# Performance work log

Hardware: AMD Instinct MI355X
Metric: run time of the kernel (lower is better)

## Reference

```python
import jax, jax.numpy as jnp
import numpy as np


def _gcn_conv(x, W, b, src, dst, deg_inv_sqrt, n_nodes):
    # x: [N, Fin], W: [Fin, Fout]; edges (with self-loops): src, dst [E+N]
    h = x @ W  # [N, Fout]
    norm = deg_inv_sqrt[src] * deg_inv_sqrt[dst]  # [E+N]
    msgs = h[src] * norm[:, None]  # gather-multiply
    out = jax.ops.segment_sum(msgs, dst, num_segments=n_nodes)  # scatter-add
    return out + b


def setup_inputs() -> dict:
    key = jax.random.key(0)
    k1, k2, k3, k4 = jax.random.split(key, 4)
    N, E, FIN, HID, OUT = 100000, 3200000, 128, 32, 32
    x = jax.random.normal(k1, (N, FIN), dtype=jnp.float32)
    edge_index = jax.random.randint(k2, (2, E), 0, N, dtype=jnp.int64)
    W1 = jax.random.normal(k3, (FIN, HID), dtype=jnp.float32) * (1.0 / np.sqrt(FIN))
    b1 = jnp.zeros((HID,), dtype=jnp.float32)
    W2 = jax.random.normal(k4, (HID, OUT), dtype=jnp.float32) * (1.0 / np.sqrt(HID))
    b2 = jnp.zeros((OUT,), dtype=jnp.float32)
    return {"x": x, "edge_index": edge_index, "W1": W1, "b1": b1, "W2": W2, "b2": b2}


def reference(x, edge_index, W1, b1, W2, b2):
    n = x.shape[0]
    # GCNConv defaults: add self-loops, symmetric normalization D^-1/2 (A+I) D^-1/2
    loops = jnp.arange(n, dtype=edge_index.dtype)
    src = jnp.concatenate([edge_index[0], loops])
    dst = jnp.concatenate([edge_index[1], loops])
    deg = jax.ops.segment_sum(jnp.ones_like(dst, dtype=x.dtype), dst, num_segments=n)
    deg_inv_sqrt = jnp.where(deg > 0, jax.lax.rsqrt(jnp.maximum(deg, 1.0)), 0.0)
    h = jax.nn.relu(_gcn_conv(x, W1, b1, src, dst, deg_inv_sqrt, n))  # hidden layer + ReLU
    out = jax.nn.relu(_gcn_conv(h, W2, b2, src, dst, deg_inv_sqrt, n))  # last layer + last_activation relu
    return out
```

## Files before the change

kernel.cpp:

```cpp
#include <hip/hip_runtime.h>
#include <hip/hip_fp16.h>

#define FIN 128
#define HID 32
#define BSHIFT 8
#define BNODES 256
#define CHUNK 4096
#define NBMAX 512
#define CAPB 8960
#define G1ROWS 64


__global__ __launch_bounds__(512) void chunk_sort_kernel(const int* __restrict__ src,
                                                         const int* __restrict__ dst,
                                                         int* __restrict__ ec,
                                                         unsigned short* __restrict__ offtT,
                                                         int E, int nb, int nchunks) {
    __shared__ int hist[NBMAX];
    __shared__ int pref[NBMAX];
    __shared__ int sorted[CHUNK];
    int c = blockIdx.x, t = threadIdx.x;
    int beg = c * CHUNK;
    int cnt = min(CHUNK, E - beg);
    for (int i = t; i < nb; i += 512) hist[i] = 0;
    __syncthreads();
    int bk[8], ent[8];
    #pragma unroll
    for (int j = 0; j < 8; ++j) {
        int i = t + j * 512;
        if (i < cnt) {
            int d = dst[beg + i];
            bk[j]  = ((unsigned)d) >> BSHIFT;
            ent[j] = src[beg + i] | ((d & (BNODES - 1)) << 24);
            atomicAdd(&hist[bk[j]], 1);
        } else bk[j] = -1;
    }
    __syncthreads();
    if (t < 64) {
        int v[8];
        int s = 0;
        #pragma unroll
        for (int j = 0; j < 8; ++j) {
            int idx = t * 8 + j;
            int h = (idx < nb) ? hist[idx] : 0;
            v[j] = s; s += h;
        }
        int run = s;
        #pragma unroll
        for (int d = 1; d < 64; d <<= 1) {
            int o = __shfl_up(run, d, 64);
            if (t >= d) run += o;
        }
        int excl = run - s;
        #pragma unroll
        for (int j = 0; j < 8; ++j) {
            int idx = t * 8 + j;
            if (idx < nb) { int p = excl + v[j]; pref[idx] = p; hist[idx] = p; }
        }
    }
    __syncthreads();
    #pragma unroll
    for (int j = 0; j < 8; ++j) {
        if (bk[j] >= 0) {
            int p = atomicAdd(&hist[bk[j]], 1);
            sorted[p] = ent[j];
        }
    }
    __syncthreads();
    for (int i = t; i < cnt; i += 512) ec[(size_t)c * CHUNK + i] = sorted[i];
    for (int i = t; i < nb; i += 512) offtT[(size_t)i * nchunks + c] = (unsigned short)pref[i];
    if (t == 0) offtT[(size_t)nb * nchunks + c] = (unsigned short)cnt;
}


__global__ __launch_bounds__(512) void bucket_build_kernel(const int* __restrict__ ec,
                                                           const unsigned short* __restrict__ offtT,
                                                           int* __restrict__ entries,
                                                           float* __restrict__ dinv,
                                                           int* __restrict__ rowbeg,
                                                           int* __restrict__ rowcnt,
                                                           int n, int nb, int nchunks, int cap) {
    __shared__ int raw[CAPB];
    __shared__ int hist[BNODES];
    __shared__ int pref[BNODES];
    __shared__ int cursor[BNODES];
    __shared__ int nfill;
    int b = blockIdx.x, t = threadIdx.x;
    if (t < BNODES) hist[t] = 0;
    if (t == 0) nfill = 0;
    __syncthreads();
    const unsigned short* r0 = offtT + (size_t)b * nchunks;
    const unsigned short* r1 = offtT + (size_t)(b + 1) * nchunks;
    int lane = t & 3;
    for (int c = (t >> 2); c < nchunks; c += 128) {
        int s = r0[c], e2 = r1[c];
        int m = e2 - s;
        if (m > 0) {
            int base;
            if (lane == 0) base = atomicAdd(&nfill, m);
            base = __shfl(base, 0, 4);
            const int* p = ec + (size_t)c * CHUNK + s;
            for (int k = lane; k < m; k += 4) {
                int e = p[k];
                if (base + k < CAPB) raw[base + k] = e;
                atomicAdd(&hist[((unsigned)e) >> 24], 1);
            }
        }
    }
    __syncthreads();
    int total = min(nfill, CAPB);
    if (t < 64) {
        int v[4];
        int s = 0;
        #pragma unroll
        for (int j = 0; j < 4; ++j) { v[j] = s; s += hist[t * 4 + j]; }
        int run = s;
        #pragma unroll
        for (int d = 1; d < 64; d <<= 1) {
            int o = __shfl_up(run, d, 64);
            if (t >= d) run += o;
        }
        int excl = run - s;
        #pragma unroll
        for (int j = 0; j < 4; ++j) {
            int idx = t * 4 + j;
            int p = excl + v[j];
            pref[idx] = p; cursor[idx] = p;
        }
    }
    __syncthreads();
    int* ep = entries + (size_t)b * cap;
    for (int i = t; i < total; i += 512) {
        int e = raw[i];
        int p = atomicAdd(&cursor[((unsigned)e) >> 24], 1);
        ep[p] = e;
    }
    int node = b * BNODES + t;
    if (t < BNODES && node < n) {
        int deg = hist[t];
        dinv[node]   = rsqrtf((float)deg + 1.0f);
        rowbeg[node] = b * cap + pref[t];
        rowcnt[node] = deg;
    }
}


__global__ __launch_bounds__(256) void gemm1_kernel(const float* __restrict__ x,
                                                    const float* __restrict__ W,
                                                    const float* __restrict__ dinv,
                                                    __half* __restrict__ h16, int n) {
    __shared__ float Ws[FIN * HID];
    int t = threadIdx.x;
    for (int i = t; i < FIN * HID; i += 256) Ws[i] = W[i];
    __syncthreads();
    int row0 = blockIdx.x * G1ROWS;
    int tr = t >> 3, tc = t & 7;
    int r0 = row0 + tr * 2, c0 = tc * 4;
    bool v0 = r0 < n, v1 = (r0 + 1) < n;
    const float* p0 = v0 ? &x[(size_t)r0 * FIN] : x;
    const float* p1 = v1 ? &x[(size_t)(r0 + 1) * FIN] : x;
    float4 a0 = make_float4(0.f, 0.f, 0.f, 0.f);
    float4 a1 = make_float4(0.f, 0.f, 0.f, 0.f);
    #pragma unroll 8
    for (int k4 = 0; k4 < FIN / 4; ++k4) {
        float4 xv0 = *(const float4*)&p0[k4 * 4];
        float4 xv1 = *(const float4*)&p1[k4 * 4];
        float4 w0 = *(const float4*)&Ws[(k4 * 4 + 0) * HID + c0];
        float4 w1 = *(const float4*)&Ws[(k4 * 4 + 1) * HID + c0];
        float4 w2 = *(const float4*)&Ws[(k4 * 4 + 2) * HID + c0];
        float4 w3 = *(const float4*)&Ws[(k4 * 4 + 3) * HID + c0];
        a0.x = fmaf(xv0.x, w0.x, a0.x); a0.y = fmaf(xv0.x, w0.y, a0.y);
        a0.z = fmaf(xv0.x, w0.z, a0.z); a0.w = fmaf(xv0.x, w0.w, a0.w);
        a0.x = fmaf(xv0.y, w1.x, a0.x); a0.y = fmaf(xv0.y, w1.y, a0.y);
        a0.z = fmaf(xv0.y, w1.z, a0.z); a0.w = fmaf(xv0.y, w1.w, a0.w);
        a0.x = fmaf(xv0.z, w2.x, a0.x); a0.y = fmaf(xv0.z, w2.y, a0.y);
        a0.z = fmaf(xv0.z, w2.z, a0.z); a0.w = fmaf(xv0.z, w2.w, a0.w);
        a0.x = fmaf(xv0.w, w3.x, a0.x); a0.y = fmaf(xv0.w, w3.y, a0.y);
        a0.z = fmaf(xv0.w, w3.z, a0.z); a0.w = fmaf(xv0.w, w3.w, a0.w);
        a1.x = fmaf(xv1.x, w0.x, a1.x); a1.y = fmaf(xv1.x, w0.y, a1.y);
        a1.z = fmaf(xv1.x, w0.z, a1.z); a1.w = fmaf(xv1.x, w0.w, a1.w);
        a1.x = fmaf(xv1.y, w1.x, a1.x); a1.y = fmaf(xv1.y, w1.y, a1.y);
        a1.z = fmaf(xv1.y, w1.z, a1.z); a1.w = fmaf(xv1.y, w1.w, a1.w);
        a1.x = fmaf(xv1.z, w2.x, a1.x); a1.y = fmaf(xv1.z, w2.y, a1.y);
        a1.z = fmaf(xv1.z, w2.z, a1.z); a1.w = fmaf(xv1.z, w2.w, a1.w);
        a1.x = fmaf(xv1.w, w3.x, a1.x); a1.y = fmaf(xv1.w, w3.y, a1.y);
        a1.z = fmaf(xv1.w, w3.z, a1.z); a1.w = fmaf(xv1.w, w3.w, a1.w);
    }
    #pragma unroll
    for (int rr = 0; rr < 2; ++rr) {
        int row = r0 + rr;
        float4 a = rr ? a1 : a0;
        float sc = (row < n) ? dinv[row] : 0.f;
        __half2 q0 = __floats2half2_rn(a.x * sc, a.y * sc);
        __half2 q1 = __floats2half2_rn(a.z * sc, a.w * sc);
        __half2* dstp = (__half2*)&h16[(size_t)row * HID + c0];
        dstp[0] = q0;
        dstp[1] = q1;
    }
}


template <int FUSEW2>
__global__ __launch_bounds__(256) void gather_kernel(const int* __restrict__ entries,
                                                     const int* __restrict__ rowbeg,
                                                     const int* __restrict__ rowcnt,
                                                     const float* __restrict__ dinv,
                                                     const __half* __restrict__ h16,
                                                     const float* __restrict__ bias,
                                                     const float* __restrict__ W2,
                                                     __half* __restrict__ houth,
                                                     float* __restrict__ outf,
                                                     int n, int sent) {
    __shared__ float Ws[HID * HID];
    int t = threadIdx.x;
    if (FUSEW2) {
        for (int i = t; i < HID * HID; i += 256) Ws[i] = W2[i];
        __syncthreads();
    }
    int g = t >> 2, f = t & 3;
    int i = blockIdx.x * 64 + g;
    if (i >= n) return;
    float di = dinv[i];
    float a[8];
    {
        float4 sv4 = *(const float4*)&h16[(size_t)i * HID + f * 8];
        const __half2* sh = (const __half2*)&sv4;
        #pragma unroll
        for (int q = 0; q < 4; ++q) {
            float2 fp = __half22float2(sh[q]);
            a[2 * q] = fp.x; a[2 * q + 1] = fp.y;
        }
    }
    int beg = rowbeg[i], cnt = rowcnt[i];
    for (int base = 0; base < cnt; base += 8) {
        int i0 = base + f, i1 = base + 4 + f;
        int sv0 = (i0 < cnt) ? entries[beg + i0] : sent;
        int sv1 = (i1 < cnt) ? entries[beg + i1] : sent;
        sv0 &= 0xFFFFFF; sv1 &= 0xFFFFFF;
        float4 hv[8];
        #pragma unroll
        for (int j = 0; j < 4; ++j) {
            int e = __shfl(sv0, j, 4);
            hv[j] = *(const float4*)&h16[(size_t)e * HID + f * 8];
        }
        #pragma unroll
        for (int j = 0; j < 4; ++j) {
            int e = __shfl(sv1, j, 4);
            hv[4 + j] = *(const float4*)&h16[(size_t)e * HID + f * 8];
        }
        #pragma unroll
        for (int j = 0; j < 8; ++j) {
            const __half2* hp = (const __half2*)&hv[j];
            #pragma unroll
            for (int q = 0; q < 4; ++q) {
                float2 fp = __half22float2(hp[q]);
                a[2 * q] += fp.x; a[2 * q + 1] += fp.y;
            }
        }
    }
    float4 b0 = *(const float4*)&bias[f * 8];
    float4 b1 = *(const float4*)&bias[f * 8 + 4];
    float bj[8] = {b0.x, b0.y, b0.z, b0.w, b1.x, b1.y, b1.z, b1.w};
    float rl[8];
    #pragma unroll
    for (int j = 0; j < 8; ++j) rl[j] = fmaxf(bj[j] + di * a[j], 0.f);

    if (!FUSEW2) {
        *(float4*)&outf[(size_t)i * HID + f * 8]     = make_float4(rl[0], rl[1], rl[2], rl[3]);
        *(float4*)&outf[(size_t)i * HID + f * 8 + 4] = make_float4(rl[4], rl[5], rl[6], rl[7]);
    } else {
        int c0 = f * 8;
        float o[8] = {0.f, 0.f, 0.f, 0.f, 0.f, 0.f, 0.f, 0.f};
        #pragma unroll
        for (int s = 0; s < 4; ++s) {
            #pragma unroll
            for (int j = 0; j < 8; ++j) {
                float av = __shfl(rl[j], s, 4);
                int k = s * 8 + j;
                float4 w0 = *(const float4*)&Ws[k * HID + c0];
                float4 w1 = *(const float4*)&Ws[k * HID + c0 + 4];
                o[0] = fmaf(av, w0.x, o[0]); o[1] = fmaf(av, w0.y, o[1]);
                o[2] = fmaf(av, w0.z, o[2]); o[3] = fmaf(av, w0.w, o[3]);
                o[4] = fmaf(av, w1.x, o[4]); o[5] = fmaf(av, w1.y, o[5]);
                o[6] = fmaf(av, w1.z, o[6]); o[7] = fmaf(av, w1.w, o[7]);
            }
        }
        float4 tmp;
        __half2* hp2 = (__half2*)&tmp;
        #pragma unroll
        for (int j = 0; j < 4; ++j) hp2[j] = __floats2half2_rn(di * o[2 * j], di * o[2 * j + 1]);
        *(float4*)&houth[(size_t)i * HID + f * 8] = tmp;
    }
}

extern "C" void kernel_launch(void* const* d_in, const int* in_sizes, int n_in,
                              void* d_out, int out_size, void* d_ws, size_t ws_size,
                              hipStream_t stream) {
    const float* x  = (const float*)d_in[0];
    const int*   ei = (const int*)d_in[1];
    const float* W1 = (const float*)d_in[2];
    const float* b1 = (const float*)d_in[3];
    const float* W2 = (const float*)d_in[4];
    const float* b2 = (const float*)d_in[5];
    float* out = (float*)d_out;

    int n = in_sizes[0] / FIN;
    int E = in_sizes[1] / 2;
    const int* src = ei;
    const int* dst = ei + E;

    int nb = (n + BNODES - 1) / BNODES;
    int nchunks = (E + CHUNK - 1) / CHUNK;
    int ggrid = (n + G1ROWS) / G1ROWS;
    int npad = ggrid * G1ROWS;
    int cap = CAPB;

    char* ws = (char*)d_ws;
    size_t off = 0;
    auto alloc = [&](size_t bytes) { char* p = ws + off; off += (bytes + 255) & ~(size_t)255; return p; };
    int*            ec      = (int*)alloc((size_t)nchunks * CHUNK * 4);
    unsigned short* offtT   = (unsigned short*)alloc((size_t)(nb + 1) * nchunks * 2);
    int*            entries = (int*)alloc((size_t)nb * cap * 4);
    float*          dinv    = (float*)alloc((size_t)n * 4);
    int*            rowbeg  = (int*)alloc((size_t)n * 4);
    int*            rowcnt  = (int*)alloc((size_t)n * 4);
    __half*         hha     = (__half*)alloc((size_t)npad * HID * 2);
    __half*         hhb     = (__half*)alloc((size_t)(n + 1) * HID * 2);

    hipMemsetAsync(hhb + (size_t)n * HID, 0, HID * 2, stream);

    chunk_sort_kernel<<<nchunks, 512, 0, stream>>>(src, dst, ec, offtT, E, nb, nchunks);
    bucket_build_kernel<<<nb, 512, 0, stream>>>(ec, offtT, entries, dinv, rowbeg, rowcnt,
                                                n, nb, nchunks, cap);

    gemm1_kernel<<<ggrid, 256, 0, stream>>>(x, W1, dinv, hha, n);
    gather_kernel<1><<<(n + 63) / 64, 256, 0, stream>>>(entries, rowbeg, rowcnt, dinv, hha,
                                                        b1, W2, hhb, nullptr, n, n);

    gather_kernel<0><<<(n + 63) / 64, 256, 0, stream>>>(entries, rowbeg, rowcnt, dinv, hhb,
                                                        b2, nullptr, nullptr, out, n, n);
}
```

Measured before the change: 248.0 us.

## Split feature matrices into 16-column half planes for cache-friendly gathers

Stores the fp16 hidden features as two separate 16-column planes and runs each gather pass once per plane, so each pass's random-access working set (about 3.2 MB per plane) is half the size and fits better in L2/MALL. Layer 1 becomes two gather passes; the second combines the stashed fp32 first-half result with its own half before applying the fused W2 projection. Layer 2 is likewise split into two passes. This trades extra kernel launches, re-reading the edge list four times instead of twice, and an fp32 intermediate buffer for better cache hit rates on the random gathers.

```diff
diff --git a/kernel.cpp b/kernel.cpp
--- a/kernel.cpp
+++ b/kernel.cpp
@@ -9,6 +9,7 @@
 #define NBMAX 512
 #define CAPB 8960
 #define G1ROWS 64
+#define PL 16
 
 
 __global__ __launch_bounds__(512) void chunk_sort_kernel(const int* __restrict__ src,
@@ -148,7 +149,8 @@
 __global__ __launch_bounds__(256) void gemm1_kernel(const float* __restrict__ x,
                                                     const float* __restrict__ W,
                                                     const float* __restrict__ dinv,
-                                                    __half* __restrict__ h16, int n) {
+                                                    __half* __restrict__ hpa,
+                                                    __half* __restrict__ hpb, int n) {
     __shared__ float Ws[FIN * HID];
     int t = threadIdx.x;
     for (int i = t; i < FIN * HID; i += 256) Ws[i] = W[i];
@@ -186,34 +188,37 @@
         a1.x = fmaf(xv1.w, w3.x, a1.x); a1.y = fmaf(xv1.w, w3.y, a1.y);
         a1.z = fmaf(xv1.w, w3.z, a1.z); a1.w = fmaf(xv1.w, w3.w, a1.w);
     }
+    __half* hp = (c0 >= PL) ? hpb : hpa;
+    int pc = c0 & (PL - 1);
     #pragma unroll
     for (int rr = 0; rr < 2; ++rr) {
         int row = r0 + rr;
         float4 a = rr ? a1 : a0;
         float sc = (row < n) ? dinv[row] : 0.f;
-        __half2 q0 = __floats2half2_rn(a.x * sc, a.y * sc);
-        __half2 q1 = __floats2half2_rn(a.z * sc, a.w * sc);
-        __half2* dstp = (__half2*)&h16[(size_t)row * HID + c0];
-        dstp[0] = q0;
-        dstp[1] = q1;
-    }
-}
-
-
-template <int FUSEW2>
+        union { __half2 h2[2]; float2 f2; } pk;
+        pk.h2[0] = __floats2half2_rn(a.x * sc, a.y * sc);
+        pk.h2[1] = __floats2half2_rn(a.z * sc, a.w * sc);
+        *(float2*)&hp[(size_t)row * PL + pc] = pk.f2;
+    }
+}
+
+
+template <int MODE>
 __global__ __launch_bounds__(256) void gather_kernel(const int* __restrict__ entries,
                                                      const int* __restrict__ rowbeg,
                                                      const int* __restrict__ rowcnt,
                                                      const float* __restrict__ dinv,
-                                                     const __half* __restrict__ h16,
-                                                     const float* __restrict__ bias,
+                                                     const __half* __restrict__ hplane,
+                                                     const float* __restrict__ bias16,
+                                                     const float* __restrict__ rA,
                                                      const float* __restrict__ W2,
-                                                     __half* __restrict__ houth,
+                                                     __half* __restrict__ opa,
+                                                     __half* __restrict__ opb,
                                                      float* __restrict__ outf,
                                                      int n, int sent) {
     __shared__ float Ws[HID * HID];
     int t = threadIdx.x;
-    if (FUSEW2) {
+    if (MODE == 1) {
         for (int i = t; i < HID * HID; i += 256) Ws[i] = W2[i];
         __syncthreads();
     }
@@ -221,75 +226,75 @@
     int i = blockIdx.x * 64 + g;
     if (i >= n) return;
     float di = dinv[i];
-    float a[8];
+    float a0, a1, a2, a3;
     {
-        float4 sv4 = *(const float4*)&h16[(size_t)i * HID + f * 8];
-        const __half2* sh = (const __half2*)&sv4;
-        #pragma unroll
-        for (int q = 0; q < 4; ++q) {
-            float2 fp = __half22float2(sh[q]);
-            a[2 * q] = fp.x; a[2 * q + 1] = fp.y;
-        }
+        float2 sv = *(const float2*)&hplane[(size_t)i * PL + f * 4];
+        const __half2* sh = (const __half2*)&sv;
+        float2 u = __half22float2(sh[0]), v = __half22float2(sh[1]);
+        a0 = u.x; a1 = u.y; a2 = v.x; a3 = v.y;
     }
     int beg = rowbeg[i], cnt = rowcnt[i];
-    for (int base = 0; base < cnt; base += 8) {
-        int i0 = base + f, i1 = base + 4 + f;
-        int sv0 = (i0 < cnt) ? entries[beg + i0] : sent;
-        int sv1 = (i1 < cnt) ? entries[beg + i1] : sent;
-        sv0 &= 0xFFFFFF; sv1 &= 0xFFFFFF;
-        float4 hv[8];
-        #pragma unroll
-        for (int j = 0; j < 4; ++j) {
-            int e = __shfl(sv0, j, 4);
-            hv[j] = *(const float4*)&h16[(size_t)e * HID + f * 8];
-        }
-        #pragma unroll
-        for (int j = 0; j < 4; ++j) {
-            int e = __shfl(sv1, j, 4);
-            hv[4 + j] = *(const float4*)&h16[(size_t)e * HID + f * 8];
-        }
-        #pragma unroll
-        for (int j = 0; j < 8; ++j) {
-            const __half2* hp = (const __half2*)&hv[j];
+    for (int base = 0; base < cnt; base += 16) {
+        int sv[4];
+        #pragma unroll
+        for (int k = 0; k < 4; ++k) {
+            int idx = base + f * 4 + k;
+            sv[k] = (idx < cnt) ? entries[beg + idx] : sent;
+        }
+        float2 hv[16];
+        #pragma unroll
+        for (int e = 0; e < 16; ++e) {
+            int en = __shfl(sv[e & 3], e >> 2, 4) & 0xFFFFFF;
+            hv[e] = *(const float2*)&hplane[(size_t)en * PL + f * 4];
+        }
+        #pragma unroll
+        for (int e = 0; e < 16; ++e) {
+            const __half2* hp = (const __half2*)&hv[e];
+            float2 u = __half22float2(hp[0]), v = __half22float2(hp[1]);
+            a0 += u.x; a1 += u.y; a2 += v.x; a3 += v.y;
+        }
+    }
+    float4 bb = *(const float4*)&bias16[f * 4];
+    float rl[4];
+    rl[0] = fmaxf(bb.x + di * a0, 0.f);
+    rl[1] = fmaxf(bb.y + di * a1, 0.f);
+    rl[2] = fmaxf(bb.z + di * a2, 0.f);
+    rl[3] = fmaxf(bb.w + di * a3, 0.f);
+
+    if (MODE == 0) {
+        *(float4*)&outf[(size_t)i * PL + f * 4] = make_float4(rl[0], rl[1], rl[2], rl[3]);
+    } else if (MODE == 2) {
+        *(float4*)&outf[(size_t)i * HID + f * 4] = make_float4(rl[0], rl[1], rl[2], rl[3]);
+    } else {
+        float r[32];
+        const float4* ra = (const float4*)&rA[(size_t)i * PL];
+        float4 ra0 = ra[0], ra1 = ra[1], ra2 = ra[2], ra3 = ra[3];
+        r[0] = ra0.x; r[1] = ra0.y; r[2]  = ra0.z; r[3]  = ra0.w;
+        r[4] = ra1.x; r[5] = ra1.y; r[6]  = ra1.z; r[7]  = ra1.w;
+        r[8] = ra2.x; r[9] = ra2.y; r[10] = ra2.z; r[11] = ra2.w;
+        r[12] = ra3.x; r[13] = ra3.y; r[14] = ra3.z; r[15] = ra3.w;
+        #pragma unroll
+        for (int s = 0; s < 4; ++s) {
             #pragma unroll
-            for (int q = 0; q < 4; ++q) {
-                float2 fp = __half22float2(hp[q]);
-                a[2 * q] += fp.x; a[2 * q + 1] += fp.y;
-            }
-        }
-    }
-    float4 b0 = *(const float4*)&bias[f * 8];
-    float4 b1 = *(const float4*)&bias[f * 8 + 4];
-    float bj[8] = {b0.x, b0.y, b0.z, b0.w, b1.x, b1.y, b1.z, b1.w};
-    float rl[8];
-    #pragma unroll
-    for (int j = 0; j < 8; ++j) rl[j] = fmaxf(bj[j] + di * a[j], 0.f);
-
-    if (!FUSEW2) {
-        *(float4*)&outf[(size_t)i * HID + f * 8]     = make_float4(rl[0], rl[1], rl[2], rl[3]);
-        *(float4*)&outf[(size_t)i * HID + f * 8 + 4] = make_float4(rl[4], rl[5], rl[6], rl[7]);
-    } else {
+            for (int j = 0; j < 4; ++j) r[16 + s * 4 + j] = __shfl(rl[j], s, 4);
+        }
         int c0 = f * 8;
         float o[8] = {0.f, 0.f, 0.f, 0.f, 0.f, 0.f, 0.f, 0.f};
         #pragma unroll
-        for (int s = 0; s < 4; ++s) {
-            #pragma unroll
-            for (int j = 0; j < 8; ++j) {
-                float av = __shfl(rl[j], s, 4);
-                int k = s * 8 + j;
-                float4 w0 = *(const float4*)&Ws[k * HID + c0];
-                float4 w1 = *(const float4*)&Ws[k * HID + c0 + 4];
-                o[0] = fmaf(av, w0.x, o[0]); o[1] = fmaf(av, w0.y, o[1]);
-                o[2] = fmaf(av, w0.z, o[2]); o[3] = fmaf(av, w0.w, o[3]);
-                o[4] = fmaf(av, w1.x, o[4]); o[5] = fmaf(av, w1.y, o[5]);
-                o[6] = fmaf(av, w1.z, o[6]); o[7] = fmaf(av, w1.w, o[7]);
-            }
-        }
-        float4 tmp;
-        __half2* hp2 = (__half2*)&tmp;
-        #pragma unroll
-        for (int j = 0; j < 4; ++j) hp2[j] = __floats2half2_rn(di * o[2 * j], di * o[2 * j + 1]);
-        *(float4*)&houth[(size_t)i * HID + f * 8] = tmp;
+        for (int k = 0; k < HID; ++k) {
+            float av = r[k];
+            float4 w0 = *(const float4*)&Ws[k * HID + c0];
+            float4 w1 = *(const float4*)&Ws[k * HID + c0 + 4];
+            o[0] = fmaf(av, w0.x, o[0]); o[1] = fmaf(av, w0.y, o[1]);
+            o[2] = fmaf(av, w0.z, o[2]); o[3] = fmaf(av, w0.w, o[3]);
+            o[4] = fmaf(av, w1.x, o[4]); o[5] = fmaf(av, w1.y, o[5]);
+            o[6] = fmaf(av, w1.z, o[6]); o[7] = fmaf(av, w1.w, o[7]);
+        }
+        __half* op = (f & 2) ? opb : opa;
+        union { __half2 h2[4]; float4 f4; } pk;
+        #pragma unroll
+        for (int j = 0; j < 4; ++j) pk.h2[j] = __floats2half2_rn(di * o[2 * j], di * o[2 * j + 1]);
+        *(float4*)&op[(size_t)i * PL + (f & 1) * 8] = pk.f4;
     }
 }
 
@@ -324,19 +329,32 @@
     float*          dinv    = (float*)alloc((size_t)n * 4);
     int*            rowbeg  = (int*)alloc((size_t)n * 4);
     int*            rowcnt  = (int*)alloc((size_t)n * 4);
-    __half*         hha     = (__half*)alloc((size_t)npad * HID * 2);
-    __half*         hhb     = (__half*)alloc((size_t)(n + 1) * HID * 2);
-
-    hipMemsetAsync(hhb + (size_t)n * HID, 0, HID * 2, stream);
+    __half*         hpa     = (__half*)alloc((size_t)npad * PL * 2);
+    __half*         hpb     = (__half*)alloc((size_t)npad * PL * 2);
+    __half*         hqa     = (__half*)alloc((size_t)(n + 1) * PL * 2);
+    __half*         hqb     = (__half*)alloc((size_t)(n + 1) * PL * 2);
+    float*          rAbuf   = (float*)alloc((size_t)n * PL * 4);
+
+    hipMemsetAsync(hqa + (size_t)n * PL, 0, PL * 2, stream);
+    hipMemsetAsync(hqb + (size_t)n * PL, 0, PL * 2, stream);
 
     chunk_sort_kernel<<<nchunks, 512, 0, stream>>>(src, dst, ec, offtT, E, nb, nchunks);
     bucket_build_kernel<<<nb, 512, 0, stream>>>(ec, offtT, entries, dinv, rowbeg, rowcnt,
                                                 n, nb, nchunks, cap);
 
-    gemm1_kernel<<<ggrid, 256, 0, stream>>>(x, W1, dinv, hha, n);
-    gather_kernel<1><<<(n + 63) / 64, 256, 0, stream>>>(entries, rowbeg, rowcnt, dinv, hha,
-                                                        b1, W2, hhb, nullptr, n, n);
-
-    gather_kernel<0><<<(n + 63) / 64, 256, 0, stream>>>(entries, rowbeg, rowcnt, dinv, hhb,
-                                                        b2, nullptr, nullptr, out, n, n);
-}
+    gemm1_kernel<<<ggrid, 256, 0, stream>>>(x, W1, dinv, hpa, hpb, n);
+
+    int ggath = (n + 63) / 64;
+    gather_kernel<0><<<ggath, 256, 0, stream>>>(entries, rowbeg, rowcnt, dinv, hpa,
+                                                b1, nullptr, nullptr, nullptr, nullptr,
+                                                rAbuf, n, n);
+    gather_kernel<1><<<ggath, 256, 0, stream>>>(entries, rowbeg, rowcnt, dinv, hpb,
+                                                b1 + PL, rAbuf, W2, hqa, hqb,
+                                                nullptr, n, n);
+    gather_kernel<2><<<ggath, 256, 0, stream>>>(entries, rowbeg, rowcnt, dinv, hqa,
+                                                b2, nullptr, nullptr, nullptr, nullptr,
+                                                out, n, n);
+    gather_kernel<2><<<ggath, 256, 0, stream>>>(entries, rowbeg, rowcnt, dinv, hqb,
+                                                b2 + PL, nullptr, nullptr, nullptr, nullptr,
+                                                out + PL, n, n);
+}
```

Result: slower. 276.6 us (+11.5%).

## Sort nodes by degree within buckets and widen gather unroll to 16 edges

Applied to the files above, without the earlier changes.

The bucket build kernel now counting-sorts the nodes of each 256-node bucket by in-degree and writes a node permutation. Both gather kernels walk nodes through that permutation, so the wavefronts in a block handle nodes of similar degree and lose less time to divergence. The gather loop also fetches 16 neighbour rows per iteration instead of 8, giving more loads in flight. The costs are an extra indirection, less contiguous output writes, and higher register pressure from the wider unroll.

```diff
diff --git a/kernel.cpp b/kernel.cpp
--- a/kernel.cpp
+++ b/kernel.cpp
@@ -9,6 +9,7 @@
 #define NBMAX 512
 #define CAPB 8960
 #define G1ROWS 64
+#define DBINS 64
 
 
 __global__ __launch_bounds__(512) void chunk_sort_kernel(const int* __restrict__ src,
@@ -79,14 +80,18 @@
                                                            float* __restrict__ dinv,
                                                            int* __restrict__ rowbeg,
                                                            int* __restrict__ rowcnt,
+                                                           int* __restrict__ nodeperm,
                                                            int n, int nb, int nchunks, int cap) {
     __shared__ int raw[CAPB];
     __shared__ int hist[BNODES];
     __shared__ int pref[BNODES];
     __shared__ int cursor[BNODES];
+    __shared__ int dhist[DBINS];
+    __shared__ int dcur[DBINS];
     __shared__ int nfill;
     int b = blockIdx.x, t = threadIdx.x;
     if (t < BNODES) hist[t] = 0;
+    if (t < DBINS) dhist[t] = 0;
     if (t == 0) nfill = 0;
     __syncthreads();
     const unsigned short* r0 = offtT + (size_t)b * nchunks;
@@ -135,12 +140,33 @@
         int p = atomicAdd(&cursor[((unsigned)e) >> 24], 1);
         ep[p] = e;
     }
-    int node = b * BNODES + t;
-    if (t < BNODES && node < n) {
-        int deg = hist[t];
-        dinv[node]   = rsqrtf((float)deg + 1.0f);
-        rowbeg[node] = b * cap + pref[t];
-        rowcnt[node] = deg;
+    int myd = -1;
+    if (t < BNODES) {
+        myd = min(hist[t], DBINS - 1);
+        atomicAdd(&dhist[myd], 1);
+    }
+    __syncthreads();
+    if (t < 64) {
+        int s = dhist[t];
+        int run = s;
+        #pragma unroll
+        for (int d = 1; d < 64; d <<= 1) {
+            int o = __shfl_up(run, d, 64);
+            if (t >= d) run += o;
+        }
+        dcur[t] = run - s;
+    }
+    __syncthreads();
+    if (t < BNODES) {
+        int node = b * BNODES + t;
+        int rank = atomicAdd(&dcur[myd], 1);
+        nodeperm[b * BNODES + rank] = (node < n) ? node : -1;
+        if (node < n) {
+            int deg = hist[t];
+            dinv[node]   = rsqrtf((float)deg + 1.0f);
+            rowbeg[node] = b * cap + pref[t];
+            rowcnt[node] = deg;
+        }
     }
 }
 
@@ -201,7 +227,8 @@
 
 
 template <int FUSEW2>
-__global__ __launch_bounds__(256) void gather_kernel(const int* __restrict__ entries,
+__global__ __launch_bounds__(256) void gather_kernel(const int* __restrict__ nodeperm,
+                                                     const int* __restrict__ entries,
                                                      const int* __restrict__ rowbeg,
                                                      const int* __restrict__ rowcnt,
                                                      const float* __restrict__ dinv,
@@ -210,7 +237,7 @@
                                                      const float* __restrict__ W2,
                                                      __half* __restrict__ houth,
                                                      float* __restrict__ outf,
-                                                     int n, int sent) {
+                                                     int sent) {
     __shared__ float Ws[HID * HID];
     int t = threadIdx.x;
     if (FUSEW2) {
@@ -218,8 +245,8 @@
         __syncthreads();
     }
     int g = t >> 2, f = t & 3;
-    int i = blockIdx.x * 64 + g;
-    if (i >= n) return;
+    int i = nodeperm[blockIdx.x * 64 + g];
+    if (i < 0) return;
     float di = dinv[i];
     float a[8];
     {
@@ -232,25 +259,22 @@
         }
     }
     int beg = rowbeg[i], cnt = rowcnt[i];
-    for (int base = 0; base < cnt; base += 8) {
-        int i0 = base + f, i1 = base + 4 + f;
-        int sv0 = (i0 < cnt) ? entries[beg + i0] : sent;
-        int sv1 = (i1 < cnt) ? entries[beg + i1] : sent;
-        sv0 &= 0xFFFFFF; sv1 &= 0xFFFFFF;
-        float4 hv[8];
-        #pragma unroll
-        for (int j = 0; j < 4; ++j) {
-            int e = __shfl(sv0, j, 4);
-            hv[j] = *(const float4*)&h16[(size_t)e * HID + f * 8];
-        }
-        #pragma unroll
-        for (int j = 0; j < 4; ++j) {
-            int e = __shfl(sv1, j, 4);
-            hv[4 + j] = *(const float4*)&h16[(size_t)e * HID + f * 8];
-        }
-        #pragma unroll
-        for (int j = 0; j < 8; ++j) {
-            const __half2* hp = (const __half2*)&hv[j];
+    for (int base = 0; base < cnt; base += 16) {
+        int sv[4];
+        #pragma unroll
+        for (int k = 0; k < 4; ++k) {
+            int idx = base + k * 4 + f;
+            sv[k] = (idx < cnt) ? entries[beg + idx] : sent;
+        }
+        float4 hv[16];
+        #pragma unroll
+        for (int e = 0; e < 16; ++e) {
+            int en = __shfl(sv[e >> 2], e & 3, 4) & 0xFFFFFF;
+            hv[e] = *(const float4*)&h16[(size_t)en * HID + f * 8];
+        }
+        #pragma unroll
+        for (int e = 0; e < 16; ++e) {
+            const __half2* hp = (const __half2*)&hv[e];
             #pragma unroll
             for (int q = 0; q < 4; ++q) {
                 float2 fp = __half22float2(hp[q]);
@@ -324,6 +348,7 @@
     float*          dinv    = (float*)alloc((size_t)n * 4);
     int*            rowbeg  = (int*)alloc((size_t)n * 4);
     int*            rowcnt  = (int*)alloc((size_t)n * 4);
+    int*            nodeperm= (int*)alloc((size_t)nb * BNODES * 4);
     __half*         hha     = (__half*)alloc((size_t)npad * HID * 2);
     __half*         hhb     = (__half*)alloc((size_t)(n + 1) * HID * 2);
 
@@ -331,12 +356,12 @@
 
     chunk_sort_kernel<<<nchunks, 512, 0, stream>>>(src, dst, ec, offtT, E, nb, nchunks);
     bucket_build_kernel<<<nb, 512, 0, stream>>>(ec, offtT, entries, dinv, rowbeg, rowcnt,
-                                                n, nb, nchunks, cap);
+                                                nodeperm, n, nb, nchunks, cap);
 
     gemm1_kernel<<<ggrid, 256, 0, stream>>>(x, W1, dinv, hha, n);
-    gather_kernel<1><<<(n + 63) / 64, 256, 0, stream>>>(entries, rowbeg, rowcnt, dinv, hha,
-                                                        b1, W2, hhb, nullptr, n, n);
-
-    gather_kernel<0><<<(n + 63) / 64, 256, 0, stream>>>(entries, rowbeg, rowcnt, dinv, hhb,
-                                                        b2, nullptr, nullptr, out, n, n);
-}
+    gather_kernel<1><<<nb * 4, 256, 0, stream>>>(nodeperm, entries, rowbeg, rowcnt, dinv, hha,
+                                                 b1, W2, hhb, nullptr, n);
+
+    gather_kernel<0><<<nb * 4, 256, 0, stream>>>(nodeperm, entries, rowbeg, rowcnt, dinv, hhb,
+                                                 b2, nullptr, nullptr, out, n);
+}
```

Result: slower. 256.3 us (+3.3%).
